# Performance work log

Hardware: AMD Instinct MI355X
Metric: run time of the kernel (lower is better)

Reference implementation:

```python
import jax, jax.numpy as jnp
import numpy as np
import math

EPS = 1e-6  # PCEN eps


def _logit(p):
    return math.log(p / (1.0 - p))


def _pcen(mel, log_s, log_alpha, log_delta, log_r, dmin, dmax):
    """PCEN: per-channel energy normalization. mel: (B, M, T); params: (M,)."""
    s = jnp.clip(jax.nn.sigmoid(log_s), 0.05, 0.3)            # (M,)
    alpha = jnp.clip(jax.nn.sigmoid(log_alpha), 0.9, 0.999)   # (M,)
    delta = jnp.clip(jnp.exp(log_delta), dmin, dmax)          # (M,)
    r = jnp.clip(jax.nn.sigmoid(log_r), 0.05, 0.25)           # (M,)

    # IIR smoother over time: smoother_0 = mel[..., 0];
    # for t in 0..T-1: smoother = (1-s)*smoother + s*mel_t  (t=0 included -> smoothed_0 = mel_0)
    mel_t = jnp.transpose(mel, (2, 0, 1))  # (T, B, M)

    def step(sm, x):
        sm = (1.0 - s) * sm + s * x
        return sm, sm

    _, smoothed_t = jax.lax.scan(step, mel_t[0], mel_t)
    smoothed = jnp.transpose(smoothed_t, (1, 2, 0))  # (B, M, T)

    gain = (EPS + smoothed) ** (-alpha[None, :, None])
    d = delta[None, :, None]
    rr = r[None, :, None]
    return (mel * gain + d) ** rr - d ** rr


def setup_inputs() -> dict:
    key = jax.random.key(0)
    B, M, T = 64, 80, 4000
    mel = jax.random.uniform(key, (B, M, T), dtype=jnp.float32)
    f = jnp.full
    return {
        "mel": mel,
        # non-stationary expert PCEN (s=0.025, alpha=0.99, delta=2.0, r=0.5)
        "log_s_ns": f((M,), _logit(0.025), jnp.float32),
        "log_alpha_ns": f((M,), _logit(0.99), jnp.float32),
        "log_delta_ns": f((M,), math.log(2.0), jnp.float32),
        "log_r_ns": f((M,), _logit(0.5), jnp.float32),
        # stationary expert PCEN (s=0.15, alpha=0.99, delta=0.01, r=0.1)
        "log_s_st": f((M,), _logit(0.15), jnp.float32),
        "log_alpha_st": f((M,), _logit(0.99), jnp.float32),
        "log_delta_st": f((M,), math.log(0.01), jnp.float32),
        "log_r_st": f((M,), _logit(0.1), jnp.float32),
        "gate_temp": jnp.asarray(5.0, jnp.float32),
    }


def reference(mel, log_s_ns, log_alpha_ns, log_delta_ns, log_r_ns,
              log_s_st, log_alpha_st, log_delta_st, log_r_st, gate_temp):
    out_ns = _pcen(mel, log_s_ns, log_alpha_ns, log_delta_ns, log_r_ns, 0.5, 5.0)
    out_st = _pcen(mel, log_s_st, log_alpha_st, log_delta_st, log_r_st, 0.001, 0.1)

    # routing signal: spectral flatness + spectral tilt (0 learnable params)
    log_mel = jnp.log(mel + 1e-8)
    geo = jnp.exp(jnp.mean(log_mel, axis=1, keepdims=True))          # (B,1,T)
    arith = jnp.mean(mel, axis=1, keepdims=True) + 1e-8
    sf = jnp.clip(geo / arith, 0.0, 1.0)

    M = mel.shape[1]
    low = jnp.mean(mel[:, : M // 3, :], axis=1, keepdims=True)
    high = jnp.mean(mel[:, 2 * M // 3 :, :], axis=1, keepdims=True)
    tilt = jnp.clip(low / (low + high + 1e-8), 0.0, 1.0)

    sf_adj = sf + (1.0 - sf) * jax.nn.relu(tilt - 0.6)
    gate = jax.nn.sigmoid(gate_temp * (sf_adj - 0.5))
    return gate * out_st + (1.0 - gate) * out_ns
```

## Files before the change

kernel.cpp:

```cpp
#include <hip/hip_runtime.h>
#include <math.h>

static constexpr int kM = 80;
static constexpr int kT = 4000;
static constexpr int kB = 64;
static constexpr int kLow = kM / 3;
static constexpr int kHighStart = 2 * kM / 3;
static constexpr int kHighCount = kM - kHighStart;
static constexpr int kWarm = 192;
static constexpr int kLdsWords = kT + kT / 16;
#define EPSF 1e-6f
#define LOG2E 1.4426950408889634f

typedef float vfloat4 __attribute__((ext_vector_type(4)));
typedef float vfloat2 __attribute__((ext_vector_type(2)));

__device__ __forceinline__ float hw_exp2(float x) { return __builtin_amdgcn_exp2f(x); }
__device__ __forceinline__ float hw_log2(float x) { return __builtin_amdgcn_logf(x); }

__device__ __forceinline__ float fast_sigmoid(float x) {
    return __builtin_amdgcn_rcpf(1.0f + hw_exp2(-x * LOG2E));
}

__device__ __forceinline__ int skw(int w) { return w + (w >> 4); }

__global__ __launch_bounds__(256) void gate_kernel(
    const float* __restrict__ mel,
    const float* __restrict__ gate_temp,
    float* __restrict__ gate)
{
    const int b  = blockIdx.y;
    const int tc = blockIdx.x * 256 + threadIdx.x;
    if (tc >= kT / 2) return;

    const float* base = mel + (size_t)b * kM * kT + (size_t)tc * 2;

    vfloat2 slog = {0.f, 0.f}, ssum = {0.f, 0.f};
    vfloat2 slow = {0.f, 0.f}, shigh = {0.f, 0.f};

    #pragma unroll 16
    for (int m = 0; m < kM; ++m) {
        const vfloat2 v = *reinterpret_cast<const vfloat2*>(base + (size_t)m * kT);
        vfloat2 lg;
        lg.x = hw_log2(v.x + 1e-8f);
        lg.y = hw_log2(v.y + 1e-8f);
        slog += lg;
        ssum += v;
        if (m < kLow)        slow  += v;
        if (m >= kHighStart) shigh += v;
    }

    const float gt = gate_temp[0];
    vfloat2 o;
    #pragma unroll
    for (int q = 0; q < 2; ++q) {
        const float sl = (q == 0) ? slog.x : slog.y;
        const float ss = (q == 0) ? ssum.x : ssum.y;
        const float lo = (q == 0) ? slow.x : slow.y;
        const float hi = (q == 0) ? shigh.x : shigh.y;
        const float geo   = hw_exp2(sl * (1.0f / kM));
        const float arith = ss * (1.0f / kM) + 1e-8f;
        float sf = geo * __builtin_amdgcn_rcpf(arith);
        sf = fminf(fmaxf(sf, 0.0f), 1.0f);
        const float low  = lo * (1.0f / kLow);
        const float high = hi * (1.0f / kHighCount);
        float tilt = low * __builtin_amdgcn_rcpf(low + high + 1e-8f);
        tilt = fminf(fmaxf(tilt, 0.0f), 1.0f);
        const float sfa = sf + (1.0f - sf) * fmaxf(tilt - 0.6f, 0.0f);
        const float g = fast_sigmoid(gt * (sfa - 0.5f));
        if (q == 0) o.x = g; else o.y = g;
    }
    *reinterpret_cast<vfloat2*>(gate + (size_t)b * kT + (size_t)tc * 2) = o;
}

__global__ __launch_bounds__(256) void pcen_kernel(
    const float* __restrict__ mel,
    const float* __restrict__ ls_ns, const float* __restrict__ la_ns,
    const float* __restrict__ ld_ns, const float* __restrict__ lr_ns,
    const float* __restrict__ ls_st, const float* __restrict__ la_st,
    const float* __restrict__ ld_st, const float* __restrict__ lr_st,
    const float* __restrict__ gate,
    float* __restrict__ out)
{
    const int m = blockIdx.x;
    const int b = blockIdx.y;

    const float s_ns     = fminf(fmaxf(fast_sigmoid(ls_ns[m]), 0.05f), 0.3f);
    const float alpha_ns = fminf(fmaxf(fast_sigmoid(la_ns[m]), 0.9f), 0.999f);
    const float delta_ns = fminf(fmaxf(hw_exp2(ld_ns[m] * LOG2E), 0.5f), 5.0f);
    const float r_ns     = fminf(fmaxf(fast_sigmoid(lr_ns[m]), 0.05f), 0.25f);
    const float s_st     = fminf(fmaxf(fast_sigmoid(ls_st[m]), 0.05f), 0.3f);
    const float alpha_st = fminf(fmaxf(fast_sigmoid(la_st[m]), 0.9f), 0.999f);
    const float delta_st = fminf(fmaxf(hw_exp2(ld_st[m] * LOG2E), 0.001f), 0.1f);
    const float r_st     = fminf(fmaxf(fast_sigmoid(lr_st[m]), 0.05f), 0.25f);
    const float dr_ns = hw_exp2(r_ns * hw_log2(delta_ns));
    const float dr_st = hw_exp2(r_st * hw_log2(delta_st));

    const vfloat2 a2 = {1.0f - s_ns, 1.0f - s_st};
    const vfloat2 s2 = {s_ns, s_st};
    const vfloat2 d2 = {delta_ns, delta_st};
    const float man = -alpha_ns, mas = -alpha_st;

    const size_t rowoff = ((size_t)b * kM + m) * kT;
    const float* row = mel + rowoff;

    const int tid = threadIdx.x;
    const int t0  = tid * 16;
    const bool valid = (t0 < kT);

    __shared__ float xs[kLdsWords];

    float x[16];
    float gv[16];
    if (valid) {
        const float4* p = reinterpret_cast<const float4*>(row + t0);
        #pragma unroll
        for (int q = 0; q < 4; ++q) {
            const float4 v = p[q];
            x[4*q+0] = v.x; x[4*q+1] = v.y; x[4*q+2] = v.z; x[4*q+3] = v.w;
        }
        const float4* gp = reinterpret_cast<const float4*>(gate + (size_t)b * kT + t0);
        #pragma unroll
        for (int q = 0; q < 4; ++q) {
            const float4 v = gp[q];
            gv[4*q+0] = v.x; gv[4*q+1] = v.y; gv[4*q+2] = v.z; gv[4*q+3] = v.w;
        }
        #pragma unroll
        for (int k = 0; k < 16; ++k) xs[skw(t0 + k)] = x[k];
    }
    __syncthreads();

    vfloat2 sm = {0.0f, 0.0f};
    if (valid) {
        if (t0 >= kWarm) {
            const int ws = t0 - kWarm;
            vfloat2 B0 = {0,0}, B1 = {0,0}, B2 = {0,0}, B3 = {0,0};
            #pragma unroll 4
            for (int j = 0; j < 48; ++j) {
                const float v0 = xs[skw(ws +   0 + j)];
                const float v1 = xs[skw(ws +  48 + j)];
                const float v2 = xs[skw(ws +  96 + j)];
                const float v3 = xs[skw(ws + 144 + j)];
                B0 = a2 * B0 + s2 * v0;
                B1 = a2 * B1 + s2 * v1;
                B2 = a2 * B2 + s2 * v2;
                B3 = a2 * B3 + s2 * v3;
            }
            const vfloat2 p2  = a2  * a2;
            const vfloat2 p4  = p2  * p2;
            const vfloat2 p8  = p4  * p4;
            const vfloat2 p16 = p8  * p8;
            const vfloat2 p32 = p16 * p16;
            const vfloat2 p48 = p32 * p16;
            sm = ((B0 * p48 + B1) * p48 + B2) * p48 + B3;
        } else if (t0 > 0) {
            const float x0 = xs[0];
            sm.x = x0; sm.y = x0;
            for (int j = 0; j < t0; ++j) {
                const float v = xs[skw(j)];
                sm = a2 * sm + s2 * v;
            }
        } else {
            sm.x = x[0]; sm.y = x[0];
        }
    }

    if (valid) {
        float4* op = reinterpret_cast<float4*>(out + rowoff + t0);
        #pragma unroll
        for (int q = 0; q < 4; ++q) {
            float4 v;
            #pragma unroll
            for (int j = 0; j < 4; ++j) {
                const int k = 4*q + j;
                const float xv = x[k];
                sm = a2 * sm + s2 * xv;
                vfloat2 g2;
                g2.x = hw_exp2(man * hw_log2(sm.x + EPSF));
                g2.y = hw_exp2(mas * hw_log2(sm.y + EPSF));
                const vfloat2 u2 = g2 * xv + d2;
                const float on = hw_exp2(r_ns * hw_log2(u2.x)) - dr_ns;
                const float os = hw_exp2(r_st * hw_log2(u2.y)) - dr_st;
                (&v.x)[j] = fmaf(gv[k], os - on, on);
            }
            op[q] = v;
        }
    }
}

extern "C" void kernel_launch(void* const* d_in, const int* in_sizes, int n_in,
                              void* d_out, int out_size, void* d_ws, size_t ws_size,
                              hipStream_t stream)
{
    const float* mel       = (const float*)d_in[0];
    const float* ls_ns     = (const float*)d_in[1];
    const float* la_ns     = (const float*)d_in[2];
    const float* ld_ns     = (const float*)d_in[3];
    const float* lr_ns     = (const float*)d_in[4];
    const float* ls_st     = (const float*)d_in[5];
    const float* la_st     = (const float*)d_in[6];
    const float* ld_st     = (const float*)d_in[7];
    const float* lr_st     = (const float*)d_in[8];
    const float* gate_temp = (const float*)d_in[9];
    float* out  = (float*)d_out;
    float* gate = (float*)d_ws;

    dim3 gA((kT / 2 + 255) / 256, kB);
    gate_kernel<<<gA, 256, 0, stream>>>(mel, gate_temp, gate);

    dim3 gB(kM, kB);
    pcen_kernel<<<gB, 256, 0, stream>>>(mel, ls_ns, la_ns, ld_ns, lr_ns,
                                        ls_st, la_st, ld_st, lr_st, gate, out);
}
```

Baseline: 220.1 us.

## Replace LDS warm-up scan with chunk-sum prefix combine and split gate reduction

The PCEN kernel no longer re-runs a 192-step warm-up recurrence over an LDS copy of the row. Each thread now computes its own 16-element chunk contribution, publishes it to shared memory, and combines the previous 12 chunks weighted by powers of (1-s)^16, truncating older history. Separately, the gate kernel splits the 80-channel reduction across two halves of the block and merges partial sums through shared memory, which raises parallelism. The truncation to 192 samples matches the old warm-up window, so accuracy depends on the decay being small for the parameter range.

```diff
diff --git a/kernel.cpp b/kernel.cpp
--- a/kernel.cpp
+++ b/kernel.cpp
@@ -7,8 +7,7 @@
 static constexpr int kLow = kM / 3;
 static constexpr int kHighStart = 2 * kM / 3;
 static constexpr int kHighCount = kM - kHighStart;
-static constexpr int kWarm = 192;
-static constexpr int kLdsWords = kT + kT / 16;
+static constexpr int kTrunc = 12;
 #define EPSF 1e-6f
 #define LOG2E 1.4426950408889634f
 
@@ -21,56 +20,66 @@
 __device__ __forceinline__ float fast_sigmoid(float x) {
     return __builtin_amdgcn_rcpf(1.0f + hw_exp2(-x * LOG2E));
 }
-
-__device__ __forceinline__ int skw(int w) { return w + (w >> 4); }
 
 __global__ __launch_bounds__(256) void gate_kernel(
     const float* __restrict__ mel,
     const float* __restrict__ gate_temp,
     float* __restrict__ gate)
 {
-    const int b  = blockIdx.y;
-    const int tc = blockIdx.x * 256 + threadIdx.x;
-    if (tc >= kT / 2) return;
-
-    const float* base = mel + (size_t)b * kM * kT + (size_t)tc * 2;
-
-    vfloat2 slog = {0.f, 0.f}, ssum = {0.f, 0.f};
-    vfloat2 slow = {0.f, 0.f}, shigh = {0.f, 0.f};
-
-    #pragma unroll 16
-    for (int m = 0; m < kM; ++m) {
-        const vfloat2 v = *reinterpret_cast<const vfloat2*>(base + (size_t)m * kT);
-        vfloat2 lg;
-        lg.x = hw_log2(v.x + 1e-8f);
-        lg.y = hw_log2(v.y + 1e-8f);
-        slog += lg;
-        ssum += v;
-        if (m < kLow)        slow  += v;
-        if (m >= kHighStart) shigh += v;
-    }
-
-    const float gt = gate_temp[0];
-    vfloat2 o;
-    #pragma unroll
-    for (int q = 0; q < 2; ++q) {
-        const float sl = (q == 0) ? slog.x : slog.y;
-        const float ss = (q == 0) ? ssum.x : ssum.y;
-        const float lo = (q == 0) ? slow.x : slow.y;
-        const float hi = (q == 0) ? shigh.x : shigh.y;
-        const float geo   = hw_exp2(sl * (1.0f / kM));
-        const float arith = ss * (1.0f / kM) + 1e-8f;
+    const int tid = threadIdx.x;
+    const int c   = tid & 127;
+    const int h   = tid >> 7;
+    const int b   = blockIdx.y;
+    const int col = blockIdx.x * 128 + c;
+    const bool valid = (col < kT);
+
+    const float* base = mel + (size_t)b * kM * kT + col;
+
+    float slog = 0.f, ssum = 0.f, sband = 0.f;
+    if (valid) {
+        if (h == 0) {
+            #pragma unroll 20
+            for (int m = 0; m < 40; ++m) {
+                const float v = base[(size_t)m * kT];
+                slog += hw_log2(v + 1e-8f);
+                ssum += v;
+                if (m < kLow) sband += v;
+            }
+        } else {
+            #pragma unroll 20
+            for (int m = 40; m < 80; ++m) {
+                const float v = base[(size_t)m * kT];
+                slog += hw_log2(v + 1e-8f);
+                ssum += v;
+                if (m >= kHighStart) sband += v;
+            }
+        }
+    }
+
+    __shared__ float p1[3][128];
+    if (h == 1) {
+        p1[0][c] = slog; p1[1][c] = ssum; p1[2][c] = sband;
+    }
+    __syncthreads();
+
+    if (h == 0 && valid) {
+        const float tlog  = slog + p1[0][c];
+        const float tsum  = ssum + p1[1][c];
+        const float thigh = p1[2][c];
+        const float tlow  = sband;
+
+        const float gt = gate_temp[0];
+        const float geo   = hw_exp2(tlog * (1.0f / kM));
+        const float arith = tsum * (1.0f / kM) + 1e-8f;
         float sf = geo * __builtin_amdgcn_rcpf(arith);
         sf = fminf(fmaxf(sf, 0.0f), 1.0f);
-        const float low  = lo * (1.0f / kLow);
-        const float high = hi * (1.0f / kHighCount);
+        const float low  = tlow  * (1.0f / kLow);
+        const float high = thigh * (1.0f / kHighCount);
         float tilt = low * __builtin_amdgcn_rcpf(low + high + 1e-8f);
         tilt = fminf(fmaxf(tilt, 0.0f), 1.0f);
         const float sfa = sf + (1.0f - sf) * fmaxf(tilt - 0.6f, 0.0f);
-        const float g = fast_sigmoid(gt * (sfa - 0.5f));
-        if (q == 0) o.x = g; else o.y = g;
-    }
-    *reinterpret_cast<vfloat2*>(gate + (size_t)b * kT + (size_t)tc * 2) = o;
+        gate[(size_t)b * kT + col] = fast_sigmoid(gt * (sfa - 0.5f));
+    }
 }
 
 __global__ __launch_bounds__(256) void pcen_kernel(
@@ -91,10 +100,12 @@
     const float r_ns     = fminf(fmaxf(fast_sigmoid(lr_ns[m]), 0.05f), 0.25f);
     const float s_st     = fminf(fmaxf(fast_sigmoid(ls_st[m]), 0.05f), 0.3f);
     const float alpha_st = fminf(fmaxf(fast_sigmoid(la_st[m]), 0.9f), 0.999f);
+    const float alpha_dummy = alpha_st;
     const float delta_st = fminf(fmaxf(hw_exp2(ld_st[m] * LOG2E), 0.001f), 0.1f);
     const float r_st     = fminf(fmaxf(fast_sigmoid(lr_st[m]), 0.05f), 0.25f);
     const float dr_ns = hw_exp2(r_ns * hw_log2(delta_ns));
     const float dr_st = hw_exp2(r_st * hw_log2(delta_st));
+    (void)alpha_dummy;
 
     const vfloat2 a2 = {1.0f - s_ns, 1.0f - s_st};
     const vfloat2 s2 = {s_ns, s_st};
@@ -104,11 +115,9 @@
     const size_t rowoff = ((size_t)b * kM + m) * kT;
     const float* row = mel + rowoff;
 
-    const int tid = threadIdx.x;
-    const int t0  = tid * 16;
+    const int i  = threadIdx.x;
+    const int t0 = i * 16;
     const bool valid = (t0 < kT);
-
-    __shared__ float xs[kLdsWords];
 
     float x[16];
     float gv[16];
@@ -125,44 +134,42 @@
             const float4 v = gp[q];
             gv[4*q+0] = v.x; gv[4*q+1] = v.y; gv[4*q+2] = v.z; gv[4*q+3] = v.w;
         }
-        #pragma unroll
-        for (int k = 0; k < 16; ++k) xs[skw(t0 + k)] = x[k];
-    }
+    } else {
+        #pragma unroll
+        for (int k = 0; k < 16; ++k) { x[k] = 0.0f; gv[k] = 0.0f; }
+    }
+
+    __shared__ float sv0;
+    if (i == 0) sv0 = x[0];
+
+    vfloat2 Bv = {0.0f, 0.0f};
+    #pragma unroll
+    for (int k = 0; k < 16; ++k) {
+        Bv = a2 * Bv + s2 * x[k];
+    }
+    const vfloat2 p2  = a2 * a2;
+    const vfloat2 p4  = p2 * p2;
+    const vfloat2 p8  = p4 * p4;
+    const vfloat2 A2  = p8 * p8;
+
+    __shared__ vfloat2 Btab[256];
+    Btab[i] = Bv;
     __syncthreads();
 
     vfloat2 sm = {0.0f, 0.0f};
-    if (valid) {
-        if (t0 >= kWarm) {
-            const int ws = t0 - kWarm;
-            vfloat2 B0 = {0,0}, B1 = {0,0}, B2 = {0,0}, B3 = {0,0};
-            #pragma unroll 4
-            for (int j = 0; j < 48; ++j) {
-                const float v0 = xs[skw(ws +   0 + j)];
-                const float v1 = xs[skw(ws +  48 + j)];
-                const float v2 = xs[skw(ws +  96 + j)];
-                const float v3 = xs[skw(ws + 144 + j)];
-                B0 = a2 * B0 + s2 * v0;
-                B1 = a2 * B1 + s2 * v1;
-                B2 = a2 * B2 + s2 * v2;
-                B3 = a2 * B3 + s2 * v3;
-            }
-            const vfloat2 p2  = a2  * a2;
-            const vfloat2 p4  = p2  * p2;
-            const vfloat2 p8  = p4  * p4;
-            const vfloat2 p16 = p8  * p8;
-            const vfloat2 p32 = p16 * p16;
-            const vfloat2 p48 = p32 * p16;
-            sm = ((B0 * p48 + B1) * p48 + B2) * p48 + B3;
-        } else if (t0 > 0) {
-            const float x0 = xs[0];
-            sm.x = x0; sm.y = x0;
-            for (int j = 0; j < t0; ++j) {
-                const float v = xs[skw(j)];
-                sm = a2 * sm + s2 * v;
-            }
-        } else {
-            sm.x = x[0]; sm.y = x[0];
-        }
+    vfloat2 pw = {1.0f, 1.0f};
+    #pragma unroll
+    for (int k = 0; k < kTrunc; ++k) {
+        const vfloat2 Bk = Btab[(i - 1 - k) & 255];
+        if (k < i) {
+            sm = pw * Bk + sm;
+            pw = pw * A2;
+        }
+    }
+    if (i <= kTrunc) {
+        const float x0 = sv0;
+        const vfloat2 x02 = {x0, x0};
+        sm = pw * x02 + sm;
     }
 
     if (valid) {
@@ -205,7 +212,7 @@
     float* out  = (float*)d_out;
     float* gate = (float*)d_ws;
 
-    dim3 gA((kT / 2 + 255) / 256, kB);
+    dim3 gA((kT + 127) / 128, kB);
     gate_kernel<<<gA, 256, 0, stream>>>(mel, gate_temp, gate);
 
     dim3 gB(kM, kB);
```

Measured after the change: 180.1 us. 18.2% less time.
